# Performance work log

Hardware: AMD Instinct MI355X
Metric: run time of the kernel (lower is better)

## Reference

```python
import jax, jax.numpy as jnp
import numpy as np

HID = 64      # HIDDEN_DIM
VOCAB = 64    # VOCAB_SIZE
INNER = 24    # INNER_DIM
SEQ = 32      # SEQ_LEN
CAP = 8       # CAPACITY_LIMIT (deque maxlen)
LR = 0.05     # INFERENCE_LR
B1, B2, EPS = 0.9, 0.999, 1e-8   # torch Adam defaults
LN_EPS = 1e-5                    # torch LayerNorm default
BATCH = 8192


def setup_inputs() -> dict:
    key = jax.random.key(0)
    ks = jax.random.split(key, 8)
    def w(k, shape, s=0.02):
        return jax.random.normal(k, shape, jnp.float32) * s
    return {
        "seqs": jax.random.randint(ks[0], (BATCH, SEQ), 0, VOCAB, dtype=jnp.int32),
        "embed": w(ks[1], (VOCAB, HID), 1.0),
        "ff_w1": w(ks[2], (HID, 2 * HID)), "ff_b1": jnp.zeros((2 * HID,), jnp.float32),
        "ff_w2": w(ks[3], (2 * HID, HID)), "ff_b2": jnp.zeros((HID,), jnp.float32),
        "ln_g": jnp.ones((HID,), jnp.float32), "ln_b": jnp.zeros((HID,), jnp.float32),
        "mlp_w1": w(ks[4], (HID, INNER), 0.1), "mlp_b1": jnp.zeros((INNER,), jnp.float32),
        "mlp_w2": w(ks[5], (INNER, HID), 0.1), "mlp_b2": jnp.zeros((HID,), jnp.float32),
        "out_w": w(ks[6], (HID, VOCAB)), "out_b": jnp.zeros((VOCAB,), jnp.float32),
    }


def _mlp(p, x):
    w1, b1, w2, b2 = p
    return jnp.maximum(x @ w1 + b1, 0.0) @ w2 + b2


def reference(seqs, embed, ff_w1, ff_b1, ff_w2, ff_b2, ln_g, ln_b,
              mlp_w1, mlp_b1, mlp_w2, mlp_b2, out_w, out_b):
    # Encoder over all tokens used (t = 0..SEQ-2), batched: [B, 31, HID]
    h = embed[seqs[:, : SEQ - 1]]
    f = jnp.maximum(h @ ff_w1 + ff_b1, 0.0) @ ff_w2 + ff_b2
    x = h + f
    mu = x.mean(-1, keepdims=True)
    var = ((x - mu) ** 2).mean(-1, keepdims=True)
    enc = ln_g * (x - mu) * jax.lax.rsqrt(var + LN_EPS) + ln_b

    # deque(maxlen=8) over pairs (t even -> key, t odd -> val) keeps last 8 pairs:
    # keys at t = 14,16,...,28 ; vals at t = 15,17,...,29. Entries are detached.
    keys = jax.lax.stop_gradient(enc[:, 14:29:2])  # [B, 8, HID]
    vals = jax.lax.stop_gradient(enc[:, 15:30:2])  # [B, 8, HID]
    q = enc[:, SEQ - 2]                            # [B, HID]

    # load_state_dict copy breaks the graph -> base MLP params are constants here
    p0 = tuple(jax.lax.stop_gradient(p) for p in (mlp_w1, mlp_b1, mlp_w2, mlp_b2))
    steps = jnp.arange(1, CAP + 1, dtype=jnp.float32)

    def per_sample(k_i, v_i, q_i):
        def adam_step(carry, kv):
            p, m, v = carry
            kh, vh, t = kv
            g = jax.grad(lambda pp: jnp.mean((_mlp(pp, kh) - vh) ** 2))(p)
            m = jax.tree_util.tree_map(lambda a, b: B1 * a + (1.0 - B1) * b, m, g)
            v = jax.tree_util.tree_map(lambda a, b: B2 * a + (1.0 - B2) * b * b, v, g)
            bc1 = 1.0 - B1 ** t
            bc2 = 1.0 - B2 ** t
            p = jax.tree_util.tree_map(
                lambda pp, mm, vv: pp - LR * (mm / bc1) / (jnp.sqrt(vv / bc2) + EPS),
                p, m, v)
            return (p, m, v), None
        zeros = jax.tree_util.tree_map(jnp.zeros_like, p0)
        (pT, _, _), _ = jax.lax.scan(adam_step, (p0, zeros, zeros), (k_i, v_i, steps))
        return _mlp(pT, q_i)

    hq = jax.vmap(per_sample)(keys, vals, q)   # [B, HID]
    return hq @ out_w + out_b                  # [B, VOCAB]
```

## Files before the change

kernel.cpp:

```cpp
#include <hip/hip_runtime.h>
#include <hip/hip_bf16.h>
#include <math.h>

#define HID   64
#define VOCABN 64
#define INNER 24
#define SEQN  32
#define CAPN  8
#define NPOS  17
#define BATCHN 8192

typedef float f32x4 __attribute__((ext_vector_type(4)));
typedef float f32x2 __attribute__((ext_vector_type(2)));

static __device__ __forceinline__ f32x4 sp4(float x) { return (f32x4){x, x, x, x}; }
static __device__ __forceinline__ f32x4 fma4(f32x4 a, f32x4 b, f32x4 c) {
  f32x4 r; r.x = fmaf(a.x, b.x, c.x); r.y = fmaf(a.y, b.y, c.y);
           r.z = fmaf(a.z, b.z, c.z); r.w = fmaf(a.w, b.w, c.w); return r;
}
static __device__ __forceinline__ f32x4 max4(f32x4 a, float b) {
  f32x4 r; r.x = fmaxf(a.x, b); r.y = fmaxf(a.y, b);
           r.z = fmaxf(a.z, b); r.w = fmaxf(a.w, b); return r;
}
static __device__ __forceinline__ f32x4 rsq4(f32x4 a) {
  f32x4 r; r.x = __builtin_amdgcn_rsqf(a.x); r.y = __builtin_amdgcn_rsqf(a.y);
           r.z = __builtin_amdgcn_rsqf(a.z); r.w = __builtin_amdgcn_rsqf(a.w); return r;
}

static __device__ const float CMSBR[8] = {
  0.01581139f, 0.01176584f, 0.01010053f, 0.00918844f,
  0.00862495f, 0.00825540f, 0.00800653f, 0.00783856f
};

template <int PAT>
static __device__ __forceinline__ float swz(float x) {
  return __int_as_float(__builtin_amdgcn_ds_swizzle(__float_as_int(x), PAT));
}

__device__ __forceinline__ float allred16q(f32x4 p) {
  float x = (p.x + p.y) + (p.z + p.w);
  int y;
  y = __builtin_amdgcn_update_dpp(__float_as_int(x), __float_as_int(x),
                                  0xB1, 0xF, 0xF, false);
  x += __int_as_float(y);
  y = __builtin_amdgcn_update_dpp(__float_as_int(x), __float_as_int(x),
                                  0x4E, 0xF, 0xF, false);
  x += __int_as_float(y);
  x += swz<0x101F>(x);
  x += swz<0x201F>(x);
  return x;
}

__global__ __launch_bounds__(128) void build_table(
    const float* __restrict__ embed,
    const float* __restrict__ ff_w1,
    const float* __restrict__ ff_b1,
    const float* __restrict__ ff_w2,
    const float* __restrict__ ff_b2,
    const float* __restrict__ ln_g,
    const float* __restrict__ ln_b,
    float* __restrict__ etab)
{
  __shared__ float h[64];
  __shared__ float A1[128];
  __shared__ float xs[64];
  const int r = blockIdx.x;
  const int t = threadIdx.x;

  if (t < 64) h[t] = embed[r * 64 + t];
  __syncthreads();

  {
    float acc = ff_b1[t];
    #pragma unroll 8
    for (int k = 0; k < 64; ++k)
      acc = fmaf(h[k], ff_w1[k * 128 + t], acc);
    A1[t] = fmaxf(acc, 0.f);
  }
  __syncthreads();

  if (t < 64) {
    float acc = ff_b2[t];
    #pragma unroll 8
    for (int k = 0; k < 128; ++k)
      acc = fmaf(A1[k], ff_w2[k * 64 + t], acc);
    xs[t] = acc + h[t];
  }
  __syncthreads();

  if (t < 64) {
    float s1 = 0.f;
    if (t < 4)
      for (int j = 0; j < 16; ++j) s1 += xs[t + 4 * j];
    s1 += __shfl_xor(s1, 1);
    s1 += __shfl_xor(s1, 2);
    s1 = __shfl(s1, 0);
    float mu = s1 * 0.015625f;

    float s2 = 0.f;
    if (t < 4)
      for (int j = 0; j < 16; ++j) {
        float d = xs[t + 4 * j] - mu;
        s2 = fmaf(d, d, s2);
      }
    s2 += __shfl_xor(s2, 1);
    s2 += __shfl_xor(s2, 2);
    s2 = __shfl(s2, 0);
    float var = s2 * 0.015625f;
    float rs  = rsqrtf(var + 1e-5f);

    etab[r * 64 + t] = fmaf((xs[t] - mu) * rs, ln_g[t], ln_b[t]);
  }
}

__device__ __forceinline__ void adam_q(f32x4& p, f32x4& m, f32x4& v,
                                       f32x4 g1, f32x4 g2, float cmsbr) {
  m = fma4(sp4(0.9f),   m, g1);
  v = fma4(sp4(0.999f), v, g2);
  f32x4 r = rsq4(max4(v, 1e-30f));
  f32x4 t = m * sp4(cmsbr);
  p = fma4(-t, r, p);
}

__global__ __launch_bounds__(256, 2) void adapt_kernel(
    const int* __restrict__ seqs,
    const float* __restrict__ etab,
    const float* __restrict__ mlp_w1,
    const float* __restrict__ mlp_b1,
    const float* __restrict__ mlp_w2,
    const float* __restrict__ mlp_b2,
    const float* __restrict__ out_w,
    const float* __restrict__ out_b,
    float* __restrict__ out)
{
  __shared__ __align__(16) float hqv[4][64];
  const int t    = threadIdx.x;
  const int wv   = t >> 6;
  const int lane = t & 63;
  const int g    = lane >> 4;
  const int u16  = lane & 15;
  const int s    = blockIdx.x * 4 + wv;
  const int off  = 6 * g;

  const int* __restrict__ srow = seqs + s * SEQN + 14;

  f32x4 w1q[6], m1q[6], v1q[6], w2q[6], m2q[6], v2q[6];
  #pragma unroll
  for (int m = 0; m < 6; ++m) {
    f32x4 a;
    a.x = mlp_w1[(4 * u16 + 0) * INNER + off + m];
    a.y = mlp_w1[(4 * u16 + 1) * INNER + off + m];
    a.z = mlp_w1[(4 * u16 + 2) * INNER + off + m];
    a.w = mlp_w1[(4 * u16 + 3) * INNER + off + m];
    w1q[m] = a;
    w2q[m] = *(const f32x4*)&mlp_w2[(off + m) * HID + 4 * u16];
    m1q[m] = sp4(0.f); v1q[m] = sp4(0.f); m2q[m] = sp4(0.f); v2q[m] = sp4(0.f);
  }
  f32x4 b1q = sp4(0.f);
  if (!(g & 1)) {
    if (u16 == 0) { b1q.x = mlp_b1[off + 0]; b1q.y = mlp_b1[off + 1];
                    b1q.z = mlp_b1[off + 2]; b1q.w = mlp_b1[off + 3]; }
    else if (u16 == 1) { b1q.x = mlp_b1[off + 4]; b1q.y = mlp_b1[off + 5]; }
  } else {
    if (u16 == 1) { b1q.z = mlp_b1[off + 0]; b1q.w = mlp_b1[off + 1]; }
    else if (u16 == 2) { b1q.x = mlp_b1[off + 2]; b1q.y = mlp_b1[off + 3];
                         b1q.z = mlp_b1[off + 4]; b1q.w = mlp_b1[off + 5]; }
  }
  f32x4 mb1 = sp4(0.f), vb1 = sp4(0.f);
  f32x4 b2q = *(const f32x4*)&mlp_b2[4 * u16];
  f32x4 mb2 = sp4(0.f), vb2 = sp4(0.f);

  const bool ge0 = !(g & 1) && (u16 == 0);
  const bool ge1 = !(g & 1) && (u16 == 1);
  const bool go1 =  (g & 1) && (u16 == 1);
  const bool go2 =  (g & 1) && (u16 == 2);
  const bool g0a = (g == 0);

  const f32x4* e4 = (const f32x4*)etab;
  f32x4 kp = e4[srow[0] * 16 + u16];
  f32x4 vp = e4[srow[1] * 16 + u16];

  #pragma unroll 2
  for (int st = 0; st < 8; ++st) {
    const float cmsbr = CMSBR[st];

    f32x4 pz[6];
    #pragma unroll
    for (int m = 0; m < 6; ++m) pz[m] = kp * w1q[m];
    pz[0].x += ge0 ? b1q.x : 0.f;  pz[0].z += go1 ? b1q.z : 0.f;
    pz[1].y += ge0 ? b1q.y : 0.f;  pz[1].w += go1 ? b1q.w : 0.f;
    pz[2].z += ge0 ? b1q.z : 0.f;  pz[2].x += go2 ? b1q.x : 0.f;
    pz[3].w += ge0 ? b1q.w : 0.f;  pz[3].y += go2 ? b1q.y : 0.f;
    pz[4].x += ge1 ? b1q.x : 0.f;  pz[4].z += go2 ? b1q.z : 0.f;
    pz[5].y += ge1 ? b1q.y : 0.f;  pz[5].w += go2 ? b1q.w : 0.f;
    float a_[6];
    #pragma unroll
    for (int m = 0; m < 6; ++m) a_[m] = allred16q(pz[m]);
    #pragma unroll
    for (int m = 0; m < 6; ++m) a_[m] = fmaxf(a_[m], 0.f);

    f32x4 yq;
    yq.x = g0a ? b2q.x : 0.f; yq.y = g0a ? b2q.y : 0.f;
    yq.z = g0a ? b2q.z : 0.f; yq.w = g0a ? b2q.w : 0.f;
    #pragma unroll
    for (int m = 0; m < 6; ++m) yq = fma4(sp4(a_[m]), w2q[m], yq);
    { f32x4 e; e.x = swz<0x401F>(yq.x); e.y = swz<0x401F>(yq.y);
               e.z = swz<0x401F>(yq.z); e.w = swz<0x401F>(yq.w);
      yq = yq + e; }
    { f32x4 e; e.x = __shfl_xor(yq.x, 32); e.y = __shfl_xor(yq.y, 32);
               e.z = __shfl_xor(yq.z, 32); e.w = __shfl_xor(yq.w, 32);
      yq = yq + e; }
    f32x4 dyq = (yq - vp) * sp4(0.03125f);

    int pp1 = 2 * st + 2; pp1 = pp1 < 16 ? pp1 : 16;
    int pp2 = 2 * st + 3; pp2 = pp2 < 16 ? pp2 : 16;
    f32x4 kn = e4[srow[pp1] * 16 + u16];
    f32x4 vn = e4[srow[pp2] * 16 + u16];

    float dz[6];
    #pragma unroll
    for (int m = 0; m < 6; ++m) dz[m] = allred16q(w2q[m] * dyq);
    #pragma unroll
    for (int m = 0; m < 6; ++m) dz[m] = (a_[m] > 0.f) ? dz[m] : 0.f;

    f32x4 k01  = kp * sp4(0.1f);
    f32x4 ksq  = (sp4(0.001f) * kp) * kp;
    f32x4 dy01 = dyq * sp4(0.1f);
    f32x4 dysq = (sp4(0.001f) * dyq) * dyq;
    #pragma unroll
    for (int m = 0; m < 6; ++m) {
      float dzs = dz[m] * dz[m];
      adam_q(w1q[m], m1q[m], v1q[m], k01 * sp4(dz[m]), ksq * sp4(dzs), cmsbr);
    }
    {
      float gg0 = ge0 ? dz[0] : ge1 ? dz[4] : dz[2];
      float gg1 = ge0 ? dz[1] : ge1 ? dz[5] : dz[3];
      float gg2 = go1 ? dz[0] : ge0 ? dz[2] : dz[4];
      float gg3 = go1 ? dz[1] : ge0 ? dz[3] : dz[5];
      f32x4 g1b; g1b.x = 0.1f * gg0; g1b.y = 0.1f * gg1;
                 g1b.z = 0.1f * gg2; g1b.w = 0.1f * gg3;
      f32x4 g2b; g2b.x = 0.001f * (gg0 * gg0); g2b.y = 0.001f * (gg1 * gg1);
                 g2b.z = 0.001f * (gg2 * gg2); g2b.w = 0.001f * (gg3 * gg3);
      adam_q(b1q, mb1, vb1, g1b, g2b, cmsbr);
    }
    #pragma unroll
    for (int m = 0; m < 6; ++m) {
      float as = a_[m] * a_[m];
      adam_q(w2q[m], m2q[m], v2q[m], dy01 * sp4(a_[m]), dysq * sp4(as), cmsbr);
    }
    adam_q(b2q, mb2, vb2, dy01, dysq, cmsbr);

    kp = kn; vp = vn;
  }

  {
    f32x4 pz[6];
    #pragma unroll
    for (int m = 0; m < 6; ++m) pz[m] = kp * w1q[m];
    pz[0].x += ge0 ? b1q.x : 0.f;  pz[0].z += go1 ? b1q.z : 0.f;
    pz[1].y += ge0 ? b1q.y : 0.f;  pz[1].w += go1 ? b1q.w : 0.f;
    pz[2].z += ge0 ? b1q.z : 0.f;  pz[2].x += go2 ? b1q.x : 0.f;
    pz[3].w += ge0 ? b1q.w : 0.f;  pz[3].y += go2 ? b1q.y : 0.f;
    pz[4].x += ge1 ? b1q.x : 0.f;  pz[4].z += go2 ? b1q.z : 0.f;
    pz[5].y += ge1 ? b1q.y : 0.f;  pz[5].w += go2 ? b1q.w : 0.f;
    float aq[6];
    #pragma unroll
    for (int m = 0; m < 6; ++m) aq[m] = fmaxf(allred16q(pz[m]), 0.f);
    f32x4 hq;
    hq.x = g0a ? b2q.x : 0.f; hq.y = g0a ? b2q.y : 0.f;
    hq.z = g0a ? b2q.z : 0.f; hq.w = g0a ? b2q.w : 0.f;
    #pragma unroll
    for (int m = 0; m < 6; ++m) hq = fma4(sp4(aq[m]), w2q[m], hq);
    { f32x4 e; e.x = swz<0x401F>(hq.x); e.y = swz<0x401F>(hq.y);
               e.z = swz<0x401F>(hq.z); e.w = swz<0x401F>(hq.w);
      hq = hq + e; }
    { f32x4 e; e.x = __shfl_xor(hq.x, 32); e.y = __shfl_xor(hq.y, 32);
               e.z = __shfl_xor(hq.z, 32); e.w = __shfl_xor(hq.w, 32);
      hq = hq + e; }
    if (g0a) ((f32x4*)hqv[wv])[u16] = hq;
  }
  __syncthreads();

  {
    float acc = out_b[lane];
    const f32x4* hv = (const f32x4*)hqv[wv];
    #pragma unroll
    for (int j4 = 0; j4 < 16; ++j4) {
      f32x4 h4 = hv[j4];
      acc = fmaf(h4.x, out_w[(4 * j4 + 0) * 64 + lane], acc);
      acc = fmaf(h4.y, out_w[(4 * j4 + 1) * 64 + lane], acc);
      acc = fmaf(h4.z, out_w[(4 * j4 + 2) * 64 + lane], acc);
      acc = fmaf(h4.w, out_w[(4 * j4 + 3) * 64 + lane], acc);
    }
    out[(size_t)s * 64 + lane] = acc;
  }
}

extern "C" void kernel_launch(void* const* d_in, const int* in_sizes, int n_in,
                              void* d_out, int out_size, void* d_ws, size_t ws_size,
                              hipStream_t stream) {
  const int*   seqs   = (const int*)d_in[0];
  const float* embed  = (const float*)d_in[1];
  const float* ff_w1  = (const float*)d_in[2];
  const float* ff_b1  = (const float*)d_in[3];
  const float* ff_w2  = (const float*)d_in[4];
  const float* ff_b2  = (const float*)d_in[5];
  const float* ln_g   = (const float*)d_in[6];
  const float* ln_b   = (const float*)d_in[7];
  const float* mlp_w1 = (const float*)d_in[8];
  const float* mlp_b1 = (const float*)d_in[9];
  const float* mlp_w2 = (const float*)d_in[10];
  const float* mlp_b2 = (const float*)d_in[11];
  const float* out_w  = (const float*)d_in[12];
  const float* out_b  = (const float*)d_in[13];

  float* etab = (float*)d_ws;

  build_table<<<64, 128, 0, stream>>>(
      embed, ff_w1, ff_b1, ff_w2, ff_b2, ln_g, ln_b, etab);
  adapt_kernel<<<BATCHN / 4, 256, 0, stream>>>(
      seqs, etab, mlp_w1, mlp_b1, mlp_w2, mlp_b2, out_w, out_b,
      (float*)d_out);
}
```

Baseline: 171.2 us.

## Remap lane layout so cross-group reductions use cheaper swizzles and permlane swaps

```diff
diff --git a/kernel.cpp b/kernel.cpp
--- a/kernel.cpp
+++ b/kernel.cpp
@@ -12,6 +12,7 @@
 
 typedef float f32x4 __attribute__((ext_vector_type(4)));
 typedef float f32x2 __attribute__((ext_vector_type(2)));
+typedef int   i32x2 __attribute__((ext_vector_type(2)));
 
 static __device__ __forceinline__ f32x4 sp4(float x) { return (f32x4){x, x, x, x}; }
 static __device__ __forceinline__ f32x4 fma4(f32x4 a, f32x4 b, f32x4 c) {
@@ -35,6 +36,34 @@
 template <int PAT>
 static __device__ __forceinline__ float swz(float x) {
   return __int_as_float(__builtin_amdgcn_ds_swizzle(__float_as_int(x), PAT));
+}
+
+#if defined(__has_builtin)
+#  if __has_builtin(__builtin_amdgcn_permlane16_swap)
+#    define HAVE_PL16 1
+#  endif
+#  if __has_builtin(__builtin_amdgcn_permlane32_swap)
+#    define HAVE_PL32 1
+#  endif
+#endif
+
+static __device__ __forceinline__ float bflyP16(float x) {
+#ifdef HAVE_PL16
+  i32x2 r = __builtin_amdgcn_permlane16_swap(__float_as_int(x),
+                                             __float_as_int(x), false, false);
+  return __int_as_float(r.x) + __int_as_float(r.y);
+#else
+  return x + swz<0x401F>(x);
+#endif
+}
+static __device__ __forceinline__ float bflyP32(float x) {
+#ifdef HAVE_PL32
+  i32x2 r = __builtin_amdgcn_permlane32_swap(__float_as_int(x),
+                                             __float_as_int(x), false, false);
+  return __int_as_float(r.x) + __int_as_float(r.y);
+#else
+  return x + __shfl_xor(x, 32);
+#endif
 }
 
 __device__ __forceinline__ float allred16q(f32x4 p) {
@@ -46,8 +75,8 @@
   y = __builtin_amdgcn_update_dpp(__float_as_int(x), __float_as_int(x),
                                   0x4E, 0xF, 0xF, false);
   x += __int_as_float(y);
-  x += swz<0x101F>(x);
-  x += swz<0x201F>(x);
+  x = bflyP16(x);
+  x = bflyP32(x);
   return x;
 }
 
@@ -137,8 +166,8 @@
   const int t    = threadIdx.x;
   const int wv   = t >> 6;
   const int lane = t & 63;
-  const int g    = lane >> 4;
-  const int u16  = lane & 15;
+  const int u16  = (lane & 3) | ((lane >> 2) & 12);
+  const int g    = (lane >> 2) & 3;
   const int s    = blockIdx.x * 4 + wv;
   const int off  = 6 * g;
 
@@ -204,11 +233,11 @@
     yq.z = g0a ? b2q.z : 0.f; yq.w = g0a ? b2q.w : 0.f;
     #pragma unroll
     for (int m = 0; m < 6; ++m) yq = fma4(sp4(a_[m]), w2q[m], yq);
-    { f32x4 e; e.x = swz<0x401F>(yq.x); e.y = swz<0x401F>(yq.y);
-               e.z = swz<0x401F>(yq.z); e.w = swz<0x401F>(yq.w);
+    { f32x4 e; e.x = swz<0x101F>(yq.x); e.y = swz<0x101F>(yq.y);
+               e.z = swz<0x101F>(yq.z); e.w = swz<0x101F>(yq.w);
       yq = yq + e; }
-    { f32x4 e; e.x = __shfl_xor(yq.x, 32); e.y = __shfl_xor(yq.y, 32);
-               e.z = __shfl_xor(yq.z, 32); e.w = __shfl_xor(yq.w, 32);
+    { f32x4 e; e.x = swz<0x201F>(yq.x); e.y = swz<0x201F>(yq.y);
+               e.z = swz<0x201F>(yq.z); e.w = swz<0x201F>(yq.w);
       yq = yq + e; }
     f32x4 dyq = (yq - vp) * sp4(0.03125f);
 
@@ -271,11 +300,11 @@
     hq.z = g0a ? b2q.z : 0.f; hq.w = g0a ? b2q.w : 0.f;
     #pragma unroll
     for (int m = 0; m < 6; ++m) hq = fma4(sp4(aq[m]), w2q[m], hq);
-    { f32x4 e; e.x = swz<0x401F>(hq.x); e.y = swz<0x401F>(hq.y);
-               e.z = swz<0x401F>(hq.z); e.w = swz<0x401F>(hq.w);
+    { f32x4 e; e.x = swz<0x101F>(hq.x); e.y = swz<0x101F>(hq.y);
+               e.z = swz<0x101F>(hq.z); e.w = swz<0x101F>(hq.w);
       hq = hq + e; }
-    { f32x4 e; e.x = __shfl_xor(hq.x, 32); e.y = __shfl_xor(hq.y, 32);
-               e.z = __shfl_xor(hq.z, 32); e.w = __shfl_xor(hq.w, 32);
+    { f32x4 e; e.x = swz<0x201F>(hq.x); e.y = swz<0x201F>(hq.y);
+               e.z = swz<0x201F>(hq.z); e.w = swz<0x201F>(hq.w);
       hq = hq + e; }
     if (g0a) ((f32x4*)hqv[wv])[u16] = hq;
   }
```

Result: slower. 174.8 us (+2.1%).
